# Kernel optimization log

Measured on AMD Instinct MI355X. Metric: run time of the kernel, lower is better.

Reference implementation:

```python
import jax, jax.numpy as jnp
import numpy as np

T, D, H, E, K = 4096, 1024, 2816, 8, 2


def setup_inputs() -> dict:
    key = jax.random.key(0)
    ks = jax.random.split(key, 5)
    s = 0.02
    return {
        "x": jax.random.normal(ks[0], (T, D), dtype=jnp.float32),
        "gate_w": jax.random.normal(ks[1], (D, E), dtype=jnp.float32) * s,
        "w1": jax.random.normal(ks[2], (E, D, H), dtype=jnp.float32) * s,
        "w2": jax.random.normal(ks[3], (E, H, D), dtype=jnp.float32) * s,
        "w3": jax.random.normal(ks[4], (E, D, H), dtype=jnp.float32) * s,
    }


def reference(x, gate_w, w1, w2, w3):
    # gate + top-k routing
    gate_logits = x @ gate_w                          # [T, E]
    topk_vals, sel = jax.lax.top_k(gate_logits, K)    # [T, K]
    topk_w = jax.nn.softmax(topk_vals.astype(jnp.float32), axis=-1).astype(x.dtype)
    # scatter top-k weights back to a dense [T, E] combine matrix
    tok = jnp.arange(x.shape[0])[:, None]             # [T, 1]
    combine = jnp.zeros(gate_logits.shape, x.dtype).at[tok, sel].set(topk_w)  # [T, E]
    # per-expert SwiGLU FFN, evaluated densely and combined with (mostly-zero) weights;
    # mathematically identical to the masked gather/scatter loop in the original.
    h = jax.nn.silu(jnp.einsum("td,edh->teh", x, w1)) * jnp.einsum("td,edh->teh", x, w3)
    expert_out = jnp.einsum("teh,ehd->ted", h, w2)    # [T, E, D]
    return jnp.einsum("ted,te->td", expert_out, combine)
```

## Files before the change

kernel.cpp:

```cpp
#include <hip/hip_runtime.h>
#include <hip/hip_bf16.h>
#include <cstdint>
#include <cstddef>


#define Tt 4096
#define Dd 1024
#define Hh 2816
#define Ee 8
#define NVT 71

typedef __bf16 bf16_t;
typedef __bf16 bf16x4 __attribute__((ext_vector_type(4)));
typedef __bf16 bf16x8 __attribute__((ext_vector_type(8)));
typedef float f32x4 __attribute__((ext_vector_type(4)));

__device__ __forceinline__ void gload16(const void* g, void* l) {
  __builtin_amdgcn_global_load_lds(
      (__attribute__((address_space(1))) void*)(void*)(uintptr_t)g,
      (__attribute__((address_space(3))) void*)l, 16, 0, 0);
}
#define WAIT_VM0() asm volatile("s_waitcnt vmcnt(0)" ::: "memory")

__global__ __launch_bounds__(256) void gate_kernel(
    const float* __restrict__ x, const float* __restrict__ gw_g,
    int* __restrict__ counts, int* __restrict__ perm, float* __restrict__ topkw,
    bf16_t* __restrict__ xb) {
  __shared__ float gw[Dd * 9];
  const int tid = threadIdx.x;
  for (int i = tid; i < Dd * Ee; i += 256) gw[(i >> 3) * 9 + (i & 7)] = gw_g[i];
  __syncthreads();
  const int tok = blockIdx.x * 32 + (tid >> 3);
  const int part = tid & 7;
  const float* xr = x + (size_t)tok * Dd;
  float acc[Ee];
#pragma unroll
  for (int e = 0; e < Ee; ++e) acc[e] = 0.f;
  for (int i = 0; i < 32; ++i) {
    const int d = i * 32 + part * 4;
    const float4 xv = *(const float4*)(xr + d);
    bf16x4 bv; bv[0] = (__bf16)xv.x; bv[1] = (__bf16)xv.y; bv[2] = (__bf16)xv.z; bv[3] = (__bf16)xv.w;
    *(bf16x4*)(xb + (size_t)tok * Dd + d) = bv;
    const float xs[4] = {xv.x, xv.y, xv.z, xv.w};
#pragma unroll
    for (int j = 0; j < 4; ++j)
#pragma unroll
      for (int e = 0; e < Ee; ++e) acc[e] += xs[j] * gw[(d + j) * 9 + e];
  }
#pragma unroll
  for (int s = 1; s < 8; s <<= 1)
#pragma unroll
    for (int e = 0; e < Ee; ++e) acc[e] += __shfl_xor(acc[e], s, 64);
  if (part == 0) {
    int i0 = 0; float v0 = acc[0];
#pragma unroll
    for (int e = 1; e < Ee; ++e) if (acc[e] > v0) { v0 = acc[e]; i0 = e; }
    int i1 = -1; float v1 = -1e30f;
#pragma unroll
    for (int e = 0; e < Ee; ++e)
      if (e != i0 && acc[e] > v1) { v1 = acc[e]; i1 = e; }
    const float w0 = 1.f / (1.f + __expf(v1 - v0));
    topkw[tok * 2 + 0] = w0;
    topkw[tok * 2 + 1] = 1.f - w0;
    const int p0 = atomicAdd(&counts[i0], 1);
    perm[i0 * Tt + p0] = tok * 2 + 0;
    const int p1 = atomicAdd(&counts[i1], 1);
    perm[i1 * Tt + p1] = tok * 2 + 1;
  }
}

__global__ void scan_kernel(const int* __restrict__ counts, int* __restrict__ offs,
                            int* __restrict__ ts) {
  if (threadIdx.x == 0) {
    int s = 0, t = 0;
    for (int e = 0; e < Ee; ++e) {
      offs[e] = s; ts[e] = t;
      s += counts[e]; t += (counts[e] + 127) >> 7;
    }
    offs[Ee] = s; ts[Ee] = t;
  }
}

__global__ __launch_bounds__(256) void prep_w_kernel(
    const float* __restrict__ w1, const float* __restrict__ w3,
    const float* __restrict__ w2, bf16_t* __restrict__ w1t,
    bf16_t* __restrict__ w3t, bf16_t* __restrict__ w2t) {
  int bid = blockIdx.x;
  const int ntile = Ee * (Dd / 64) * (Hh / 64);
  const float* src; bf16_t* dst; int R, C;
  if (bid < ntile) { src = w1; dst = w1t; R = Dd; C = Hh; }
  else if (bid < 2 * ntile) { src = w3; dst = w3t; R = Dd; C = Hh; bid -= ntile; }
  else { src = w2; dst = w2t; R = Hh; C = Dd; bid -= 2 * ntile; }
  const int tilesC = C / 64, tilesR = R / 64;
  const int e = bid / (tilesR * tilesC);
  const int rem = bid % (tilesR * tilesC);
  const int r0 = (rem / tilesC) * 64, c0 = (rem % tilesC) * 64;
  src += (size_t)e * R * C;
  dst += (size_t)e * R * C;

  __shared__ bf16_t tile[64 * 68];
  const int tid = threadIdx.x;
#pragma unroll
  for (int i = 0; i < 16; ++i) {
    const int r = (tid >> 6) + i * 4;
    const int c = tid & 63;
    tile[c * 68 + r] = (__bf16)src[(size_t)(r0 + r) * C + c0 + c];
  }
  __syncthreads();
#pragma unroll
  for (int i = 0; i < 4; ++i) {
    const int c = i * 16 + (tid >> 4);
    const int rch = (tid & 15) * 4;
    uint2 val;
    val.x = *(const uint32_t*)(tile + c * 68 + rch);
    val.y = *(const uint32_t*)(tile + c * 68 + rch + 2);
    *(uint2*)(dst + (size_t)(c0 + c) * R + r0 + rch) = val;
  }
}


__global__ __launch_bounds__(256, 3) void gemm1_kernel(
    const bf16_t* __restrict__ xb, const bf16_t* __restrict__ w1t,
    const int* __restrict__ perm, const int* __restrict__ counts,
    const int* __restrict__ offs, const int* __restrict__ ts,
    bf16_t* __restrict__ g1) {
  const int G = (Hh / 128) * NVT;
  const int orig = blockIdx.x;
  const int xcd = orig & 7, seq = orig >> 3;
  const int q = G >> 3, r = G & 7;
  const int lin = (xcd < r ? xcd * (q + 1) : r * (q + 1) + (xcd - r) * q) + seq;
  const int vt = lin % NVT;
  const int nb = lin / NVT;
  if (vt >= ts[Ee]) return;
  int e = 0;
#pragma unroll
  for (int i = 1; i < Ee; ++i) if (vt >= ts[i]) e = i;
  const int ne = counts[e];
  const int m0 = (vt - ts[e]) * 128;
  const int h0 = nb * 128;
  const int hb = offs[e];

  __shared__ __align__(16) bf16_t As[128 * 64];
  __shared__ __align__(16) bf16_t Bs[128 * 64];

  const int tid = threadIdx.x;
  const int lane = tid & 63;
  const int wid = tid >> 6;
  const int scol = ((tid & 7) << 3) ^ (((tid >> 3) & 7) << 3);
  uint32_t aoff[4], boff[4];
#pragma unroll
  for (int i = 0; i < 4; ++i) {
    const int row = i * 32 + (tid >> 3);
    const int gr = m0 + row;
    const int rec = (gr < ne) ? perm[e * Tt + gr] : 0;
    aoff[i] = (uint32_t)((rec >> 1) * Dd + scol);
    boff[i] = (uint32_t)((h0 + row) * Dd + scol);
  }
  const bf16_t* w1e = w1t + (size_t)e * Hh * Dd;

  f32x4 acc[4][4];
#pragma unroll
  for (int m = 0; m < 4; ++m)
#pragma unroll
    for (int n = 0; n < 4; ++n) acc[m][n] = (f32x4){0.f, 0.f, 0.f, 0.f};

  const int wm = wid >> 1, wn = wid & 1;
  int aoffm[4], boffn[4], koff[2];
#pragma unroll
  for (int m = 0; m < 4; ++m) aoffm[m] = (wm * 64 + m * 16 + (lane & 15)) * 64;
#pragma unroll
  for (int n = 0; n < 4; ++n) boffn[n] = (wn * 64 + n * 16 + (lane & 15)) * 64;
#pragma unroll
  for (int kk = 0; kk < 2; ++kk)
    koff[kk] = (kk * 32 + (lane >> 4) * 8) ^ ((lane & 7) << 3);

  for (int kt = 0; kt < Dd / 64; ++kt) {
    const int d0 = kt * 64;
    __syncthreads();
#pragma unroll
    for (int i = 0; i < 4; ++i) {
      const int lb = (i * 256 + tid) * 8;
      gload16(xb + aoff[i] + d0, As + lb);
      gload16(w1e + boff[i] + d0, Bs + lb);
    }
    WAIT_VM0();
    __syncthreads();
#pragma unroll
    for (int kk = 0; kk < 2; ++kk) {
      bf16x8 a[4], b[4];
#pragma unroll
      for (int m = 0; m < 4; ++m) a[m] = *(const bf16x8*)(As + aoffm[m] + koff[kk]);
#pragma unroll
      for (int n = 0; n < 4; ++n) b[n] = *(const bf16x8*)(Bs + boffn[n] + koff[kk]);
#pragma unroll
      for (int m = 0; m < 4; ++m)
#pragma unroll
        for (int n = 0; n < 4; ++n)
          acc[m][n] = __builtin_amdgcn_mfma_f32_16x16x32_bf16(a[m], b[n], acc[m][n], 0, 0, 0);
    }
  }

#pragma unroll
  for (int m = 0; m < 4; ++m) {
    const int rb = m0 + wm * 64 + m * 16 + ((lane >> 4) << 2);
#pragma unroll
    for (int r2 = 0; r2 < 4; ++r2) {
      const int gr = rb + r2;
      if (gr >= ne) continue;
      bf16_t* orow = g1 + (size_t)(hb + gr) * Hh + h0 + wn * 64 + (lane & 15);
#pragma unroll
      for (int n = 0; n < 4; ++n) {
        const float v1 = acc[m][n][r2];
        orow[n * 16] = (__bf16)(v1 / (1.f + __expf(-v1)));
      }
    }
  }
}

__global__ __launch_bounds__(256, 3) void gemm2_kernel(
    const bf16_t* __restrict__ xb, const bf16_t* __restrict__ w3t,
    const int* __restrict__ perm, const int* __restrict__ counts,
    const int* __restrict__ offs, const int* __restrict__ ts,
    const bf16_t* __restrict__ g1, bf16_t* __restrict__ hbuf) {
  const int G = (Hh / 128) * NVT;
  const int orig = blockIdx.x;
  const int xcd = orig & 7, seq = orig >> 3;
  const int q = G >> 3, r = G & 7;
  const int lin = (xcd < r ? xcd * (q + 1) : r * (q + 1) + (xcd - r) * q) + seq;
  const int vt = lin % NVT;
  const int nb = lin / NVT;
  if (vt >= ts[Ee]) return;
  int e = 0;
#pragma unroll
  for (int i = 1; i < Ee; ++i) if (vt >= ts[i]) e = i;
  const int ne = counts[e];
  const int m0 = (vt - ts[e]) * 128;
  const int h0 = nb * 128;
  const int hb = offs[e];

  __shared__ __align__(16) bf16_t As[128 * 64];
  __shared__ __align__(16) bf16_t Bs[128 * 64];

  const int tid = threadIdx.x;
  const int lane = tid & 63;
  const int wid = tid >> 6;
  const int scol = ((tid & 7) << 3) ^ (((tid >> 3) & 7) << 3);
  uint32_t aoff[4], boff[4];
#pragma unroll
  for (int i = 0; i < 4; ++i) {
    const int row = i * 32 + (tid >> 3);
    const int gr = m0 + row;
    const int rec = (gr < ne) ? perm[e * Tt + gr] : 0;
    aoff[i] = (uint32_t)((rec >> 1) * Dd + scol);
    boff[i] = (uint32_t)((h0 + row) * Dd + scol);
  }
  const bf16_t* w3e = w3t + (size_t)e * Hh * Dd;

  f32x4 acc[4][4];
#pragma unroll
  for (int m = 0; m < 4; ++m)
#pragma unroll
    for (int n = 0; n < 4; ++n) acc[m][n] = (f32x4){0.f, 0.f, 0.f, 0.f};

  const int wm = wid >> 1, wn = wid & 1;
  int aoffm[4], boffn[4], koff[2];
#pragma unroll
  for (int m = 0; m < 4; ++m) aoffm[m] = (wm * 64 + m * 16 + (lane & 15)) * 64;
#pragma unroll
  for (int n = 0; n < 4; ++n) boffn[n] = (wn * 64 + n * 16 + (lane & 15)) * 64;
#pragma unroll
  for (int kk = 0; kk < 2; ++kk)
    koff[kk] = (kk * 32 + (lane >> 4) * 8) ^ ((lane & 7) << 3);

  for (int kt = 0; kt < Dd / 64; ++kt) {
    const int d0 = kt * 64;
    __syncthreads();
#pragma unroll
    for (int i = 0; i < 4; ++i) {
      const int lb = (i * 256 + tid) * 8;
      gload16(xb + aoff[i] + d0, As + lb);
      gload16(w3e + boff[i] + d0, Bs + lb);
    }
    WAIT_VM0();
    __syncthreads();
#pragma unroll
    for (int kk = 0; kk < 2; ++kk) {
      bf16x8 a[4], b[4];
#pragma unroll
      for (int m = 0; m < 4; ++m) a[m] = *(const bf16x8*)(As + aoffm[m] + koff[kk]);
#pragma unroll
      for (int n = 0; n < 4; ++n) b[n] = *(const bf16x8*)(Bs + boffn[n] + koff[kk]);
#pragma unroll
      for (int m = 0; m < 4; ++m)
#pragma unroll
        for (int n = 0; n < 4; ++n)
          acc[m][n] = __builtin_amdgcn_mfma_f32_16x16x32_bf16(a[m], b[n], acc[m][n], 0, 0, 0);
    }
  }

#pragma unroll
  for (int m = 0; m < 4; ++m) {
    const int rb = m0 + wm * 64 + m * 16 + ((lane >> 4) << 2);
#pragma unroll
    for (int r2 = 0; r2 < 4; ++r2) {
      const int gr = rb + r2;
      if (gr >= ne) continue;
      const size_t rowb = (size_t)(hb + gr) * Hh + h0 + wn * 64 + (lane & 15);
      const bf16_t* grow = g1 + rowb;
      bf16_t* hrow = hbuf + rowb;
#pragma unroll
      for (int n = 0; n < 4; ++n) {
        const float v3 = acc[m][n][r2];
        const float s = (float)grow[n * 16];
        hrow[n * 16] = (__bf16)(s * v3);
      }
    }
  }
}

__global__ __launch_bounds__(256, 3) void ffn2_kernel(
    const bf16_t* __restrict__ hbuf, const bf16_t* __restrict__ w2t,
    const int* __restrict__ perm, const int* __restrict__ counts,
    const int* __restrict__ offs, const int* __restrict__ ts,
    const float* __restrict__ topkw, float* __restrict__ obuf) {
  const int G = (Dd / 128) * NVT;
  const int orig = blockIdx.x;
  const int xcd = orig & 7, seq = orig >> 3;
  const int q = G >> 3, r = G & 7;
  const int lin = (xcd < r ? xcd * (q + 1) : r * (q + 1) + (xcd - r) * q) + seq;
  const int vt = lin % NVT;
  const int nb = lin / NVT;
  if (vt >= ts[Ee]) return;
  int e = 0;
#pragma unroll
  for (int i = 1; i < Ee; ++i) if (vt >= ts[i]) e = i;
  const int ne = counts[e];
  const int m0 = (vt - ts[e]) * 128;
  const int n0 = nb * 128;
  const int hb = offs[e];

  __shared__ __align__(16) bf16_t As[128 * 64];
  __shared__ __align__(16) bf16_t Bs[128 * 64];

  const int tid = threadIdx.x;
  const int lane = tid & 63;
  const int wid = tid >> 6;
  const int scol = ((tid & 7) << 3) ^ (((tid >> 3) & 7) << 3);
  uint32_t aoff[4], boff[4];
#pragma unroll
  for (int i = 0; i < 4; ++i) {
    const int row = i * 32 + (tid >> 3);
    int ar = hb + m0 + row;
    if (ar > 2 * Tt - 1) ar = 2 * Tt - 1;
    aoff[i] = (uint32_t)(ar * Hh + scol);
    boff[i] = (uint32_t)((n0 + row) * Hh + scol);
  }
  const bf16_t* w2e = w2t + (size_t)e * Dd * Hh;

  f32x4 acc[4][4];
#pragma unroll
  for (int m = 0; m < 4; ++m)
#pragma unroll
    for (int n = 0; n < 4; ++n) acc[m][n] = (f32x4){0.f, 0.f, 0.f, 0.f};

  const int wm = wid >> 1, wn = wid & 1;
  int aoffm[4], boffn[4], koff[2];
#pragma unroll
  for (int m = 0; m < 4; ++m) aoffm[m] = (wm * 64 + m * 16 + (lane & 15)) * 64;
#pragma unroll
  for (int n = 0; n < 4; ++n) boffn[n] = (wn * 64 + n * 16 + (lane & 15)) * 64;
#pragma unroll
  for (int kk = 0; kk < 2; ++kk)
    koff[kk] = (kk * 32 + (lane >> 4) * 8) ^ ((lane & 7) << 3);

  for (int kt = 0; kt < Hh / 64; ++kt) {
    const int k0 = kt * 64;
    __syncthreads();
#pragma unroll
    for (int i = 0; i < 4; ++i) {
      const int lb = (i * 256 + tid) * 8;
      gload16(hbuf + aoff[i] + k0, As + lb);
      gload16(w2e + boff[i] + k0, Bs + lb);
    }
    WAIT_VM0();
    __syncthreads();
#pragma unroll
    for (int kk = 0; kk < 2; ++kk) {
      bf16x8 a[4], b[4];
#pragma unroll
      for (int m = 0; m < 4; ++m) a[m] = *(const bf16x8*)(As + aoffm[m] + koff[kk]);
#pragma unroll
      for (int n = 0; n < 4; ++n) b[n] = *(const bf16x8*)(Bs + boffn[n] + koff[kk]);
#pragma unroll
      for (int m = 0; m < 4; ++m)
#pragma unroll
        for (int n = 0; n < 4; ++n)
          acc[m][n] = __builtin_amdgcn_mfma_f32_16x16x32_bf16(a[m], b[n], acc[m][n], 0, 0, 0);
    }
  }

#pragma unroll
  for (int m = 0; m < 4; ++m) {
    const int rb = m0 + wm * 64 + m * 16 + ((lane >> 4) << 2);
#pragma unroll
    for (int r2 = 0; r2 < 4; ++r2) {
      const int gr = rb + r2;
      if (gr >= ne) continue;
      const int rec = perm[e * Tt + gr];
      const float wgt = topkw[rec];
      float* orow = obuf + (size_t)rec * Dd + n0 + wn * 64 + (lane & 15);
#pragma unroll
      for (int n = 0; n < 4; ++n) orow[n * 16] = wgt * acc[m][n][r2];
    }
  }
}

__global__ __launch_bounds__(256) void combine_kernel(const float* __restrict__ obuf,
                                                      float* __restrict__ out) {
  const int t = blockIdx.x;
  const int d = threadIdx.x * 4;
  const float4 a = *(const float4*)(obuf + (size_t)(2 * t) * Dd + d);
  const float4 b = *(const float4*)(obuf + (size_t)(2 * t + 1) * Dd + d);
  float4 o;
  o.x = a.x + b.x; o.y = a.y + b.y; o.z = a.z + b.z; o.w = a.w + b.w;
  *(float4*)(out + (size_t)t * Dd + d) = o;
}

extern "C" void kernel_launch(void* const* d_in, const int* in_sizes, int n_in,
                              void* d_out, int out_size, void* d_ws, size_t ws_size,
                              hipStream_t stream) {
  const float* x = (const float*)d_in[0];
  const float* gate_w = (const float*)d_in[1];
  const float* w1 = (const float*)d_in[2];
  const float* w2 = (const float*)d_in[3];
  const float* w3 = (const float*)d_in[4];
  float* out = (float*)d_out;

  char* ws = (char*)d_ws;
  size_t off = 0;
  auto alloc = [&](size_t b) { size_t r = off; off += (b + 255) & ~(size_t)255; return r; };
  float* topkw   = (float*)(ws + alloc((size_t)Tt * 2 * 4));
  int* counts    = (int*)(ws + alloc(Ee * 4));
  int* offs      = (int*)(ws + alloc((Ee + 1) * 4));
  int* ts        = (int*)(ws + alloc((Ee + 1) * 4));
  int* perm      = (int*)(ws + alloc((size_t)Ee * Tt * 4));
  bf16_t* xb     = (bf16_t*)(ws + alloc((size_t)Tt * Dd * 2));
  const size_t w1t_off = alloc((size_t)Ee * Hh * Dd * 2);
  bf16_t* w1t    = (bf16_t*)(ws + w1t_off);
  bf16_t* w3t    = (bf16_t*)(ws + alloc((size_t)Ee * Hh * Dd * 2));
  bf16_t* w2t    = (bf16_t*)(ws + alloc((size_t)Ee * Dd * Hh * 2));
  const size_t g1_off = alloc((size_t)Tt * 2 * Hh * 2);
  bf16_t* g1     = (bf16_t*)(ws + g1_off);
  bf16_t* hbuf   = (bf16_t*)(ws + w1t_off);
  float* obuf    = (float*)(ws + g1_off);
  if (ws_size < off) return;

  hipMemsetAsync(counts, 0, Ee * 4, stream);
  gate_kernel<<<Tt / 32, 256, 0, stream>>>(x, gate_w, counts, perm, topkw, xb);
  scan_kernel<<<1, 64, 0, stream>>>(counts, offs, ts);
  prep_w_kernel<<<3 * Ee * (Dd / 64) * (Hh / 64), 256, 0, stream>>>(w1, w3, w2, w1t, w3t, w2t);
  gemm1_kernel<<<(Hh / 128) * NVT, 256, 0, stream>>>(xb, w1t, perm, counts, offs, ts, g1);
  gemm2_kernel<<<(Hh / 128) * NVT, 256, 0, stream>>>(xb, w3t, perm, counts, offs, ts, g1, hbuf);
  ffn2_kernel<<<(Dd / 128) * NVT, 256, 0, stream>>>(hbuf, w2t, perm, counts, offs, ts, topkw, obuf);
  combine_kernel<<<Tt, 256, 0, stream>>>(obuf, out);
}
```

Baseline: 361.6 us.

## Fuse w1 and w3 GEMMs into one kernel sharing the A tile

Merges the separate w1 and w3 expert GEMMs into a single 512-thread kernel. It loads the gathered token tile once and computes both projections together, with the w3 results passed through shared memory to the waves that apply SiLU and the product. This removes one full reload of the activations, the intermediate g1 write and read, and one kernel launch. Separately, the weight transpose/convert kernel now uses float4 loads and 16-byte stores. The cost is a larger block with more shared memory (48KB) and an extra LDS exchange, which may lower occupancy.

```diff
diff --git a/kernel.cpp b/kernel.cpp
--- a/kernel.cpp
+++ b/kernel.cpp
@@ -100,30 +100,34 @@
 
   __shared__ bf16_t tile[64 * 68];
   const int tid = threadIdx.x;
-#pragma unroll
-  for (int i = 0; i < 16; ++i) {
-    const int r = (tid >> 6) + i * 4;
-    const int c = tid & 63;
-    tile[c * 68 + r] = (__bf16)src[(size_t)(r0 + r) * C + c0 + c];
+  const int rr0 = tid >> 4;
+  const int c4 = (tid & 15) * 4;
+#pragma unroll
+  for (int i = 0; i < 4; ++i) {
+    const int r = rr0 + i * 16;
+    const float4 v = *(const float4*)(src + (size_t)(r0 + r) * C + c0 + c4);
+    tile[(c4 + 0) * 68 + r] = (__bf16)v.x;
+    tile[(c4 + 1) * 68 + r] = (__bf16)v.y;
+    tile[(c4 + 2) * 68 + r] = (__bf16)v.z;
+    tile[(c4 + 3) * 68 + r] = (__bf16)v.w;
   }
   __syncthreads();
-#pragma unroll
-  for (int i = 0; i < 4; ++i) {
-    const int c = i * 16 + (tid >> 4);
-    const int rch = (tid & 15) * 4;
-    uint2 val;
-    val.x = *(const uint32_t*)(tile + c * 68 + rch);
-    val.y = *(const uint32_t*)(tile + c * 68 + rch + 2);
-    *(uint2*)(dst + (size_t)(c0 + c) * R + r0 + rch) = val;
-  }
-}
-
-
-__global__ __launch_bounds__(256, 3) void gemm1_kernel(
+  const int rch = (tid & 7) * 8;
+#pragma unroll
+  for (int i = 0; i < 2; ++i) {
+    const int c = (tid >> 3) + i * 32;
+    const uint2 lo = *(const uint2*)(tile + c * 68 + rch);
+    const uint2 hi = *(const uint2*)(tile + c * 68 + rch + 4);
+    uint4 val; val.x = lo.x; val.y = lo.y; val.z = hi.x; val.w = hi.y;
+    *(uint4*)(dst + (size_t)(c0 + c) * R + r0 + rch) = val;
+  }
+}
+
+__global__ __launch_bounds__(512, 6) void ffn1_kernel(
     const bf16_t* __restrict__ xb, const bf16_t* __restrict__ w1t,
-    const int* __restrict__ perm, const int* __restrict__ counts,
-    const int* __restrict__ offs, const int* __restrict__ ts,
-    bf16_t* __restrict__ g1) {
+    const bf16_t* __restrict__ w3t, const int* __restrict__ perm,
+    const int* __restrict__ counts, const int* __restrict__ offs,
+    const int* __restrict__ ts, bf16_t* __restrict__ hbuf) {
   const int G = (Hh / 128) * NVT;
   const int orig = blockIdx.x;
   const int xcd = orig & 7, seq = orig >> 3;
@@ -141,22 +145,33 @@
   const int hb = offs[e];
 
   __shared__ __align__(16) bf16_t As[128 * 64];
-  __shared__ __align__(16) bf16_t Bs[128 * 64];
+  __shared__ __align__(16) bf16_t Bs[256 * 64];
 
   const int tid = threadIdx.x;
   const int lane = tid & 63;
   const int wid = tid >> 6;
+  const int wm = wid >> 2, wn = wid & 3;
+
   const int scol = ((tid & 7) << 3) ^ (((tid >> 3) & 7) << 3);
-  uint32_t aoff[4], boff[4];
-#pragma unroll
-  for (int i = 0; i < 4; ++i) {
-    const int row = i * 32 + (tid >> 3);
-    const int gr = m0 + row;
-    const int rec = (gr < ne) ? perm[e * Tt + gr] : 0;
-    aoff[i] = (uint32_t)((rec >> 1) * Dd + scol);
-    boff[i] = (uint32_t)((h0 + row) * Dd + scol);
-  }
-  const bf16_t* w1e = w1t + (size_t)e * Hh * Dd;
+  uint32_t aofs[2];
+  const bf16_t* bsrc[4];
+  {
+    const bf16_t* w1e = w1t + (size_t)e * Hh * Dd;
+    const bf16_t* w3e = w3t + (size_t)e * Hh * Dd;
+#pragma unroll
+    for (int i = 0; i < 2; ++i) {
+      const int row = i * 64 + (tid >> 3);
+      const int gr = m0 + row;
+      const int rec = (gr < ne) ? perm[e * Tt + gr] : 0;
+      aofs[i] = (uint32_t)((rec >> 1) * Dd + scol);
+    }
+#pragma unroll
+    for (int i = 0; i < 4; ++i) {
+      const int row = i * 64 + (tid >> 3);
+      const int hrow = h0 + (row & 127);
+      bsrc[i] = (row < 128 ? w1e : w3e) + (size_t)hrow * Dd + scol;
+    }
+  }
 
   f32x4 acc[4][4];
 #pragma unroll
@@ -164,7 +179,6 @@
 #pragma unroll
     for (int n = 0; n < 4; ++n) acc[m][n] = (f32x4){0.f, 0.f, 0.f, 0.f};
 
-  const int wm = wid >> 1, wn = wid & 1;
   int aoffm[4], boffn[4], koff[2];
 #pragma unroll
   for (int m = 0; m < 4; ++m) aoffm[m] = (wm * 64 + m * 16 + (lane & 15)) * 64;
@@ -178,11 +192,9 @@
     const int d0 = kt * 64;
     __syncthreads();
 #pragma unroll
-    for (int i = 0; i < 4; ++i) {
-      const int lb = (i * 256 + tid) * 8;
-      gload16(xb + aoff[i] + d0, As + lb);
-      gload16(w1e + boff[i] + d0, Bs + lb);
-    }
+    for (int i = 0; i < 2; ++i) gload16(xb + aofs[i] + d0, As + (i * 512 + tid) * 8);
+#pragma unroll
+    for (int i = 0; i < 4; ++i) gload16(bsrc[i] + d0, Bs + (i * 512 + tid) * 8);
     WAIT_VM0();
     __syncthreads();
 #pragma unroll
@@ -200,119 +212,38 @@
     }
   }
 
-#pragma unroll
-  for (int m = 0; m < 4; ++m) {
-    const int rb = m0 + wm * 64 + m * 16 + ((lane >> 4) << 2);
-#pragma unroll
-    for (int r2 = 0; r2 < 4; ++r2) {
-      const int gr = rb + r2;
-      if (gr >= ne) continue;
-      bf16_t* orow = g1 + (size_t)(hb + gr) * Hh + h0 + wn * 64 + (lane & 15);
-#pragma unroll
-      for (int n = 0; n < 4; ++n) {
-        const float v1 = acc[m][n][r2];
-        orow[n * 16] = (__bf16)(v1 / (1.f + __expf(-v1)));
-      }
-    }
-  }
-}
-
-__global__ __launch_bounds__(256, 3) void gemm2_kernel(
-    const bf16_t* __restrict__ xb, const bf16_t* __restrict__ w3t,
-    const int* __restrict__ perm, const int* __restrict__ counts,
-    const int* __restrict__ offs, const int* __restrict__ ts,
-    const bf16_t* __restrict__ g1, bf16_t* __restrict__ hbuf) {
-  const int G = (Hh / 128) * NVT;
-  const int orig = blockIdx.x;
-  const int xcd = orig & 7, seq = orig >> 3;
-  const int q = G >> 3, r = G & 7;
-  const int lin = (xcd < r ? xcd * (q + 1) : r * (q + 1) + (xcd - r) * q) + seq;
-  const int vt = lin % NVT;
-  const int nb = lin / NVT;
-  if (vt >= ts[Ee]) return;
-  int e = 0;
-#pragma unroll
-  for (int i = 1; i < Ee; ++i) if (vt >= ts[i]) e = i;
-  const int ne = counts[e];
-  const int m0 = (vt - ts[e]) * 128;
-  const int h0 = nb * 128;
-  const int hb = offs[e];
-
-  __shared__ __align__(16) bf16_t As[128 * 64];
-  __shared__ __align__(16) bf16_t Bs[128 * 64];
-
-  const int tid = threadIdx.x;
-  const int lane = tid & 63;
-  const int wid = tid >> 6;
-  const int scol = ((tid & 7) << 3) ^ (((tid >> 3) & 7) << 3);
-  uint32_t aoff[4], boff[4];
-#pragma unroll
-  for (int i = 0; i < 4; ++i) {
-    const int row = i * 32 + (tid >> 3);
-    const int gr = m0 + row;
-    const int rec = (gr < ne) ? perm[e * Tt + gr] : 0;
-    aoff[i] = (uint32_t)((rec >> 1) * Dd + scol);
-    boff[i] = (uint32_t)((h0 + row) * Dd + scol);
-  }
-  const bf16_t* w3e = w3t + (size_t)e * Hh * Dd;
-
-  f32x4 acc[4][4];
-#pragma unroll
-  for (int m = 0; m < 4; ++m)
-#pragma unroll
-    for (int n = 0; n < 4; ++n) acc[m][n] = (f32x4){0.f, 0.f, 0.f, 0.f};
-
-  const int wm = wid >> 1, wn = wid & 1;
-  int aoffm[4], boffn[4], koff[2];
-#pragma unroll
-  for (int m = 0; m < 4; ++m) aoffm[m] = (wm * 64 + m * 16 + (lane & 15)) * 64;
-#pragma unroll
-  for (int n = 0; n < 4; ++n) boffn[n] = (wn * 64 + n * 16 + (lane & 15)) * 64;
-#pragma unroll
-  for (int kk = 0; kk < 2; ++kk)
-    koff[kk] = (kk * 32 + (lane >> 4) * 8) ^ ((lane & 7) << 3);
-
-  for (int kt = 0; kt < Dd / 64; ++kt) {
-    const int d0 = kt * 64;
-    __syncthreads();
-#pragma unroll
-    for (int i = 0; i < 4; ++i) {
-      const int lb = (i * 256 + tid) * 8;
-      gload16(xb + aoff[i] + d0, As + lb);
-      gload16(w3e + boff[i] + d0, Bs + lb);
-    }
-    WAIT_VM0();
-    __syncthreads();
-#pragma unroll
-    for (int kk = 0; kk < 2; ++kk) {
-      bf16x8 a[4], b[4];
-#pragma unroll
-      for (int m = 0; m < 4; ++m) a[m] = *(const bf16x8*)(As + aoffm[m] + koff[kk]);
-#pragma unroll
-      for (int n = 0; n < 4; ++n) b[n] = *(const bf16x8*)(Bs + boffn[n] + koff[kk]);
-#pragma unroll
-      for (int m = 0; m < 4; ++m)
-#pragma unroll
-        for (int n = 0; n < 4; ++n)
-          acc[m][n] = __builtin_amdgcn_mfma_f32_16x16x32_bf16(a[m], b[n], acc[m][n], 0, 0, 0);
-    }
-  }
-
-#pragma unroll
-  for (int m = 0; m < 4; ++m) {
-    const int rb = m0 + wm * 64 + m * 16 + ((lane >> 4) << 2);
-#pragma unroll
-    for (int r2 = 0; r2 < 4; ++r2) {
-      const int gr = rb + r2;
-      if (gr >= ne) continue;
-      const size_t rowb = (size_t)(hb + gr) * Hh + h0 + wn * 64 + (lane & 15);
-      const bf16_t* grow = g1 + rowb;
-      bf16_t* hrow = hbuf + rowb;
-#pragma unroll
-      for (int n = 0; n < 4; ++n) {
-        const float v3 = acc[m][n][r2];
-        const float s = (float)grow[n * 16];
-        hrow[n * 16] = (__bf16)(s * v3);
+  __syncthreads();
+  bf16_t* xch = Bs;
+  if (wn >= 2) {
+#pragma unroll
+    for (int m = 0; m < 4; ++m)
+#pragma unroll
+      for (int n = 0; n < 4; ++n)
+#pragma unroll
+        for (int r2 = 0; r2 < 4; ++r2) {
+          const int row = wm * 64 + m * 16 + ((lane >> 4) << 2) + r2;
+          const int col = (wn - 2) * 64 + n * 16 + (lane & 15);
+          xch[row * 128 + (col ^ ((row & 3) << 2))] = (__bf16)acc[m][n][r2];
+        }
+  }
+  __syncthreads();
+  if (wn < 2) {
+#pragma unroll
+    for (int m = 0; m < 4; ++m) {
+#pragma unroll
+      for (int r2 = 0; r2 < 4; ++r2) {
+        const int row = wm * 64 + m * 16 + ((lane >> 4) << 2) + r2;
+        const int gr = m0 + row;
+        if (gr >= ne) continue;
+        bf16_t* orow = hbuf + (size_t)(hb + gr) * Hh + h0 + wn * 64 + (lane & 15);
+#pragma unroll
+        for (int n = 0; n < 4; ++n) {
+          const int col = wn * 64 + n * 16 + (lane & 15);
+          const float v3 = (float)xch[row * 128 + (col ^ ((row & 3) << 2))];
+          const float v1 = acc[m][n][r2];
+          const float s = v1 / (1.f + __expf(-v1));
+          orow[n * 16] = (__bf16)(s * v3);
+        }
       }
     }
   }
@@ -449,18 +380,15 @@
   bf16_t* w1t    = (bf16_t*)(ws + w1t_off);
   bf16_t* w3t    = (bf16_t*)(ws + alloc((size_t)Ee * Hh * Dd * 2));
   bf16_t* w2t    = (bf16_t*)(ws + alloc((size_t)Ee * Dd * Hh * 2));
-  const size_t g1_off = alloc((size_t)Tt * 2 * Hh * 2);
-  bf16_t* g1     = (bf16_t*)(ws + g1_off);
-  bf16_t* hbuf   = (bf16_t*)(ws + w1t_off);
-  float* obuf    = (float*)(ws + g1_off);
+  bf16_t* hbuf   = (bf16_t*)(ws + alloc((size_t)Tt * 2 * Hh * 2));
+  float* obuf    = (float*)(ws + w1t_off);
   if (ws_size < off) return;
 
   hipMemsetAsync(counts, 0, Ee * 4, stream);
   gate_kernel<<<Tt / 32, 256, 0, stream>>>(x, gate_w, counts, perm, topkw, xb);
   scan_kernel<<<1, 64, 0, stream>>>(counts, offs, ts);
   prep_w_kernel<<<3 * Ee * (Dd / 64) * (Hh / 64), 256, 0, stream>>>(w1, w3, w2, w1t, w3t, w2t);
-  gemm1_kernel<<<(Hh / 128) * NVT, 256, 0, stream>>>(xb, w1t, perm, counts, offs, ts, g1);
-  gemm2_kernel<<<(Hh / 128) * NVT, 256, 0, stream>>>(xb, w3t, perm, counts, offs, ts, g1, hbuf);
+  ffn1_kernel<<<(Hh / 128) * NVT, 512, 0, stream>>>(xb, w1t, w3t, perm, counts, offs, ts, hbuf);
   ffn2_kernel<<<(Dd / 128) * NVT, 256, 0, stream>>>(hbuf, w2t, perm, counts, offs, ts, topkw, obuf);
   combine_kernel<<<Tt, 256, 0, stream>>>(obuf, out);
 }
```

After: 1.201 ms. +232.1%, slower.
